# Kernel tuning notes

Hardware: AMD Instinct MI355X
Metric: run time of the kernel (lower is better)

The kernel has to match this reference:

```python
import jax, jax.numpy as jnp
import numpy as np

B, S, E, H = 2, 2048, 1024, 16
D = E // H  # head_dim = 64
NEG = -1e10


def setup_inputs() -> dict:
    key = jax.random.key(0)
    ks = jax.random.split(key, 12)
    sc = 1.0 / np.sqrt(E)
    return {
        "query": jax.random.normal(ks[0], (B, S, E), jnp.float32),
        "key_": jax.random.normal(ks[1], (B, S, E), jnp.float32),
        "value": jax.random.normal(ks[2], (B, S, E), jnp.float32),
        "mask": jax.random.randint(ks[3], (B, S), 0, 2, jnp.int32),
        "Wq": jax.random.normal(ks[4], (E, E), jnp.float32) * sc,
        "bq": jnp.zeros((E,), jnp.float32),
        "Wk": jax.random.normal(ks[5], (E, E), jnp.float32) * sc,
        "bk": jnp.zeros((E,), jnp.float32),
        "Wv": jax.random.normal(ks[6], (E, E), jnp.float32) * sc,
        "bv": jnp.zeros((E,), jnp.float32),
        "Wo": jax.random.normal(ks[7], (E, E), jnp.float32) * sc,
        "bo": jnp.zeros((E,), jnp.float32),
    }


def reference(query, key_, value, mask, Wq, bq, Wk, bk, Wv, bv, Wo, bo):
    # Linear projections (torch Linear: x @ W^T + b)
    Q = (query @ Wq.T + bq).reshape(B, S, H, D)
    K = (key_ @ Wk.T + bk).reshape(B, S, H, D)
    V = (value @ Wv.T + bv).reshape(B, S, H, D)
    # [B, H, Sq, Sk] scores
    scores = jnp.einsum("bqhd,bkhd->bhqk", Q, K) / jnp.sqrt(jnp.float32(D))
    # Original sets rows of masked query positions AND columns of masked key
    # positions to -1e10 (set, not add; overlapping assignment is same value).
    pad = (mask == 0)  # [B, S]
    bad = pad[:, :, None] | pad[:, None, :]  # [B, Sq, Sk]
    scores = scores + jnp.where(bad, NEG, 0.0)[:, None, :, :]
    weights = jax.nn.softmax(scores, axis=-1)
    out = jnp.einsum("bhqk,bkhd->bqhd", weights, V).reshape(B, S, E)
    return out @ Wo.T + bo
```

## Files before the change

### kernel.cpp

```cpp
#include <hip/hip_runtime.h>

typedef __attribute__((ext_vector_type(4)))  float          f32x4;
typedef __attribute__((ext_vector_type(16))) float          f32x16;
typedef __attribute__((ext_vector_type(8)))  short          s16x8;
typedef __attribute__((ext_vector_type(4)))  unsigned short u16x4;
typedef __attribute__((ext_vector_type(8)))  unsigned short u16x8;

#define MFMA_BF16(a, b, c) __builtin_amdgcn_mfma_f32_16x16x32_bf16((a), (b), (c), 0, 0, 0)
#define MFMA32(a, b, c)    __builtin_amdgcn_mfma_f32_32x32x16_bf16((a), (b), (c), 0, 0, 0)

static constexpr int Bb = 2, Ss = 2048, Ee = 1024, Hh = 16, Dd = 64;
static constexpr size_t M4 = 4u * 1024 * 1024;
static constexpr size_t M1 = 1024 * 1024;

__device__ __forceinline__ unsigned short f2b(float f) {
    unsigned u = __builtin_bit_cast(unsigned, f);
    u += 0x7fffu + ((u >> 16) & 1u);
    return (unsigned short)(u >> 16);
}

__device__ __forceinline__ void gld_lds16(const unsigned short* g, unsigned short* l) {
    __builtin_amdgcn_global_load_lds(
        (const __attribute__((address_space(1))) unsigned int*)g,
        (__attribute__((address_space(3))) unsigned int*)l, 16, 0, 0);
}

struct CvtArgs { const float* src[7]; unsigned short* dst;
                 const int* mask; float* maskf; };

__global__ __launch_bounds__(256) void cvt_bf16(CvtArgs a)
{
    if (blockIdx.x == 8192) {
#pragma unroll
        for (int j = 0; j < 16; j++) {
            int idx = threadIdx.x + j * 256;
            a.maskf[idx] = a.mask[idx] ? 1.f : 0.f;
        }
        return;
    }
    size_t i = ((size_t)blockIdx.x * 256 + threadIdx.x) * 8;
    int seg; size_t off;
    if (i < 3 * M4) { seg = (int)(i / M4);     off = i % M4; }
    else            { size_t j = i - 3 * M4;
                      seg = 3 + (int)(j / M1); off = j % M1; }
    const float* s = a.src[seg] + off;
    f32x4 x0 = *(const f32x4*)s;
    f32x4 x1 = *(const f32x4*)(s + 4);
    u16x8 o = (u16x8){f2b(x0[0]), f2b(x0[1]), f2b(x0[2]), f2b(x0[3]),
                      f2b(x1[0]), f2b(x1[1]), f2b(x1[2]), f2b(x1[3])};
    *(u16x8*)(a.dst + i) = o;
}

template <int OUT_MODE>
__device__ __forceinline__ void gemm_bf16_body(const unsigned short* __restrict__ A,
                                               const unsigned short* __restrict__ W,
                                               const float* __restrict__ bias,
                                               void* __restrict__ Cv,
                                               int m0, int n0)
{
    __shared__ __align__(16) unsigned short Al[128 * 32];
    __shared__ __align__(16) unsigned short Bl[128 * 32];

    const int tid  = threadIdx.x;
    const int lane = tid & 63;
    const int wid  = tid >> 6;
    const int quad = lane >> 4;
    const int lr   = lane & 15;
    const int wr   = (wid >> 1) * 64;
    const int wc   = (wid & 1) * 64;

    const int srow = wid * 32 + (lane >> 2);
    const int sk8  = (lane & 3) * 8;
    const unsigned short* gA = A + (size_t)(m0 + srow) * 1024 + sk8;
    const unsigned short* gW = W + (size_t)(n0 + srow) * 1024 + sk8;
    unsigned short* lA = &Al[wid * 1024];
    unsigned short* lW = &Bl[wid * 1024];

    f32x4 acc[4][4];
#pragma unroll
    for (int i = 0; i < 4; i++)
#pragma unroll
        for (int j = 0; j < 4; j++) acc[i][j] = (f32x4){0.f, 0.f, 0.f, 0.f};

    for (int ks = 0; ks < 1024; ks += 32) {
        __syncthreads();
        gld_lds16(gA + ks,              lA);
        gld_lds16(gA + ks + 16 * 1024,  lA + 512);
        gld_lds16(gW + ks,              lW);
        gld_lds16(gW + ks + 16 * 1024,  lW + 512);
        __syncthreads();

        s16x8 af[4], bf[4];
#pragma unroll
        for (int t = 0; t < 4; t++) {
            af[t] = *(const s16x8*)&Al[(wr + t * 16 + lr) * 32 + quad * 8];
            bf[t] = *(const s16x8*)&Bl[(wc + t * 16 + lr) * 32 + quad * 8];
        }
#pragma unroll
        for (int mt = 0; mt < 4; mt++)
#pragma unroll
            for (int nt = 0; nt < 4; nt++)
                acc[mt][nt] = MFMA_BF16(af[mt], bf[nt], acc[mt][nt]);
    }

#pragma unroll
    for (int mt = 0; mt < 4; mt++)
#pragma unroll
        for (int nt = 0; nt < 4; nt++) {
            int   col  = n0 + wc + nt * 16 + lr;
            float bcol = bias[col];
            int   rbase = m0 + wr + mt * 16 + quad * 4;
            if (OUT_MODE == 2) {
                int bb = rbase >> 11, s = rbase & 2047;
                u16x4 pk;
#pragma unroll
                for (int r = 0; r < 4; r++) pk[r] = f2b(acc[mt][nt][r] + bcol);
                *(u16x4*)&((unsigned short*)Cv)[((size_t)(bb * 1024 + col)) * 2048 + s] = pk;
            } else {
#pragma unroll
                for (int r = 0; r < 4; r++) {
                    float v = acc[mt][nt][r] + bcol;
                    if (OUT_MODE == 3) v *= 0.180336884f;
                    ((unsigned short*)Cv)[(size_t)(rbase + r) * 1024 + col] = f2b(v);
                }
            }
        }
}

struct GArgs {
    const unsigned short* A[3];
    const unsigned short* W[3];
    const float* bias[3];
    unsigned short* C[3];
};

__global__ __launch_bounds__(256) void proj_gemm(GArgs ga)
{
    const int id  = blockIdx.x;
    const int xcd = id & 7;
    const int t   = id >> 3;
    const int z   = t >> 5;
    const int tt  = t & 31;
    const int n0  = (tt & 7) * 128;
    const int m0  = (xcd * 4 + (tt >> 3)) * 128;

    if (z == 2)      gemm_bf16_body<2>(ga.A[2], ga.W[2], ga.bias[2], ga.C[2], m0, n0);
    else if (z == 1) gemm_bf16_body<1>(ga.A[1], ga.W[1], ga.bias[1], ga.C[1], m0, n0);
    else             gemm_bf16_body<3>(ga.A[0], ga.W[0], ga.bias[0], ga.C[0], m0, n0);
}

__global__ __launch_bounds__(256)
void out_gemm(const unsigned short* __restrict__ A,
              const unsigned short* __restrict__ W,
              const float* __restrict__ bias,
              float* __restrict__ C)
{
    __shared__ __align__(16) unsigned short Al[128 * 32];
    __shared__ __align__(16) unsigned short Bl[64 * 32];

    const int id  = blockIdx.x;
    const int xcd = id & 7;
    const int t   = id >> 3;
    const int n0  = (t & 15) * 64;
    const int m0  = (xcd * 4 + (t >> 4)) * 128;

    const int tid  = threadIdx.x;
    const int lane = tid & 63;
    const int wid  = tid >> 6;
    const int quad = lane >> 4;
    const int lr   = lane & 15;
    const int wr   = (wid >> 1) * 64;
    const int wc   = (wid & 1) * 32;

    const int srowA = wid * 32 + (lane >> 2);
    const int srowW = wid * 16 + (lane >> 2);
    const int sk8   = (lane & 3) * 8;
    const unsigned short* gA = A + (size_t)(m0 + srowA) * 1024 + sk8;
    const unsigned short* gW = W + (size_t)(n0 + srowW) * 1024 + sk8;
    unsigned short* lA = &Al[wid * 1024];
    unsigned short* lW = &Bl[wid * 512];

    f32x4 acc[4][2];
#pragma unroll
    for (int i = 0; i < 4; i++)
#pragma unroll
        for (int j = 0; j < 2; j++) acc[i][j] = (f32x4){0.f, 0.f, 0.f, 0.f};

    for (int ks = 0; ks < 1024; ks += 32) {
        __syncthreads();
        gld_lds16(gA + ks,              lA);
        gld_lds16(gA + ks + 16 * 1024,  lA + 512);
        gld_lds16(gW + ks,              lW);
        __syncthreads();

        s16x8 af[4], bf[2];
#pragma unroll
        for (int mt = 0; mt < 4; mt++)
            af[mt] = *(const s16x8*)&Al[(wr + mt * 16 + lr) * 32 + quad * 8];
#pragma unroll
        for (int nt = 0; nt < 2; nt++)
            bf[nt] = *(const s16x8*)&Bl[(wc + nt * 16 + lr) * 32 + quad * 8];
#pragma unroll
        for (int mt = 0; mt < 4; mt++)
#pragma unroll
            for (int nt = 0; nt < 2; nt++)
                acc[mt][nt] = MFMA_BF16(af[mt], bf[nt], acc[mt][nt]);
    }

#pragma unroll
    for (int mt = 0; mt < 4; mt++)
#pragma unroll
        for (int nt = 0; nt < 2; nt++) {
            int   col  = n0 + wc + nt * 16 + lr;
            float bcol = bias[col];
            int   rbase = m0 + wr + mt * 16 + quad * 4;
#pragma unroll
            for (int r = 0; r < 4; r++)
                C[(size_t)(rbase + r) * 1024 + col] = acc[mt][nt][r] + bcol;
        }
}

__global__ __launch_bounds__(256)
void flash_attn(const unsigned short* __restrict__ Q,
                const unsigned short* __restrict__ K,
                const unsigned short* __restrict__ Vt,
                const float* __restrict__ maskf,
                unsigned short* __restrict__ O)
{
    constexpr int   ST  = 76;
    constexpr float EPS = 9.31322575e-10f;
    __shared__ __align__(16) unsigned short Kl[64 * ST];
    __shared__ __align__(16) unsigned short Vl[64 * ST];
    __shared__ __align__(16) unsigned short Pl[64 * ST];
    __shared__ float lsq[4][32];

    const int id    = blockIdx.x;
    const int xcd   = id & 7;
    const int local = id >> 3;
    const int pair  = xcd * 4 + (local >> 5);
    const int b     = pair >> 4;
    const int h     = pair & 15;
    const int q0    = (local & 31) * 64;

    const int tid  = threadIdx.x;
    const int lane = tid & 63;
    const int wid  = tid >> 6;
    const int l31  = lane & 31;
    const int hl   = lane >> 5;
    const int qh   = wid & 1;
    const int kh   = wid >> 1;

    const unsigned short* qg =
        Q + (size_t)(b * 2048 + q0 + qh * 32 + l31) * 1024 + h * 64 + hl * 8;
    s16x8 qf[4];
#pragma unroll
    for (int db = 0; db < 4; db++) qf[db] = *(const s16x8*)(qg + db * 16);

    const float  mq  = maskf[b * 2048 + q0 + qh * 32 + l31];
    const float* mkp = maskf + b * 2048;

    const int lk = (tid >> 3) * ST + (tid & 7) * 8;
    const unsigned short* gK = K  + (size_t)(b * 2048 + (tid >> 3)) * 1024 + h * 64 + (tid & 7) * 8;
    const unsigned short* gV = Vt + (size_t)(b * 1024 + h * 64 + (tid >> 3)) * 2048 + (tid & 7) * 8;

    float  lsum = 0.f;
    f32x16 accO = (f32x16){0.f,0.f,0.f,0.f,0.f,0.f,0.f,0.f,
                           0.f,0.f,0.f,0.f,0.f,0.f,0.f,0.f};

    for (int kt = 0; kt < 2048; kt += 64) {
        __syncthreads();
        *(u16x8*)&Kl[lk]           = *(const u16x8*)(gK + (size_t)kt * 1024);
        *(u16x8*)&Kl[lk + 32 * ST] = *(const u16x8*)(gK + (size_t)(kt + 32) * 1024);
        *(u16x8*)&Vl[lk]           = *(const u16x8*)(gV + kt);
        *(u16x8*)&Vl[lk + 32 * ST] = *(const u16x8*)(gV + kt + (size_t)32 * 2048);
        __syncthreads();

        f32x16 st = (f32x16){0.f,0.f,0.f,0.f,0.f,0.f,0.f,0.f,
                             0.f,0.f,0.f,0.f,0.f,0.f,0.f,0.f};
#pragma unroll
        for (int db = 0; db < 4; db++) {
            s16x8 kf = *(const s16x8*)&Kl[(kh * 32 + l31) * ST + db * 16 + hl * 8];
            st = MFMA32(kf, qf[db], st);
        }
#pragma unroll
        for (int rq = 0; rq < 4; rq++) {
            int   kb = 4 * hl + 8 * rq;
            f32x4 m4 = *(const f32x4*)&mkp[kt + kh * 32 + kb];
            unsigned u[4];
#pragma unroll
            for (int r = 0; r < 4; r++) {
                float e = __builtin_amdgcn_exp2f(st[rq * 4 + r]);
                float p = e * (m4[r] * mq) + EPS;
                lsum += p;
                u[r] = __builtin_bit_cast(unsigned, p) + 0x8000u;
            }
            uint2 w;
            w.x = __builtin_amdgcn_perm(u[1], u[0], 0x07060302u);
            w.y = __builtin_amdgcn_perm(u[3], u[2], 0x07060302u);
            *(uint2*)&Pl[(qh * 32 + l31) * ST + kh * 32 + kb] = w;
        }
        __syncthreads();

#pragma unroll
        for (int ks = 0; ks < 4; ks++) {
            s16x8 pf = *(const s16x8*)&Pl[(qh * 32 + l31) * ST + ks * 16 + hl * 8];
            s16x8 vf = *(const s16x8*)&Vl[(kh * 32 + l31) * ST + ks * 16 + hl * 8];
            accO = MFMA32(pf, vf, accO);
        }
    }

    lsum += __shfl_xor(lsum, 32, 64);
    lsq[wid][l31] = lsum;
    __syncthreads();

#pragma unroll
    for (int rq = 0; rq < 4; rq++) {
        int   qr = 4 * hl + 8 * rq;
        f32x4 lA = *(const f32x4*)&lsq[qh][qr];
        f32x4 lB = *(const f32x4*)&lsq[qh + 2][qr];
#pragma unroll
        for (int r = 0; r < 4; r++) {
            float val = accO[rq * 4 + r] * __builtin_amdgcn_rcpf(lA[r] + lB[r]);
            O[(size_t)(b * 2048 + q0 + qh * 32 + qr + r) * 1024 + h * 64 +
              kh * 32 + l31] = f2b(val);
        }
    }
}

extern "C" void kernel_launch(void* const* d_in, const int* in_sizes, int n_in,
                              void* d_out, int out_size, void* d_ws, size_t ws_size,
                              hipStream_t stream)
{
    const float* query = (const float*)d_in[0];
    const float* key_  = (const float*)d_in[1];
    const float* value = (const float*)d_in[2];
    const int*   mask  = (const int*)d_in[3];
    const float* Wq    = (const float*)d_in[4];
    const float* bq    = (const float*)d_in[5];
    const float* Wk    = (const float*)d_in[6];
    const float* bk    = (const float*)d_in[7];
    const float* Wv    = (const float*)d_in[8];
    const float* bv    = (const float*)d_in[9];
    const float* Wo    = (const float*)d_in[10];
    const float* bo    = (const float*)d_in[11];
    float* out = (float*)d_out;

    unsigned short* cvt = (unsigned short*)d_ws;
    unsigned short* Aq  = cvt;
    unsigned short* Ak  = cvt + M4;
    unsigned short* Av  = cvt + 2 * M4;
    unsigned short* Wqb = cvt + 3 * M4;
    unsigned short* Wkb = Wqb + M1;
    unsigned short* Wvb = Wkb + M1;
    unsigned short* Wob = Wvb + M1;
    unsigned short* Qb  = Wob + M1;
    unsigned short* Kb  = Qb + M4;
    unsigned short* Vt  = Kb + M4;
    unsigned short* Ab  = Vt + M4;
    float*          mkf = (float*)(Ab + M4);

    CvtArgs ca;
    ca.src[0] = query; ca.src[1] = key_; ca.src[2] = value;
    ca.src[3] = Wq; ca.src[4] = Wk; ca.src[5] = Wv; ca.src[6] = Wo;
    ca.dst = cvt; ca.mask = mask; ca.maskf = mkf;
    cvt_bf16<<<dim3(8193), 256, 0, stream>>>(ca);

    GArgs ga;
    ga.A[0] = Aq;  ga.A[1] = Ak;  ga.A[2] = Av;
    ga.W[0] = Wqb; ga.W[1] = Wkb; ga.W[2] = Wvb;
    ga.bias[0] = bq; ga.bias[1] = bk; ga.bias[2] = bv;
    ga.C[0] = Qb; ga.C[1] = Kb; ga.C[2] = Vt;
    proj_gemm<<<dim3(768), 256, 0, stream>>>(ga);

    flash_attn<<<dim3(1024), 256, 0, stream>>>(Qb, Kb, Vt, mkf, Ab);
    out_gemm<<<dim3(512), 256, 0, stream>>>(Ab, Wob, bo, out);
}
```

Measured before the change: 234.7 us.

## Load K/V attention fragments directly from global into registers, bypassing LDS

```diff
diff --git a/kernel.cpp b/kernel.cpp
--- a/kernel.cpp
+++ b/kernel.cpp
@@ -229,8 +229,6 @@
 {
     constexpr int   ST  = 76;
     constexpr float EPS = 9.31322575e-10f;
-    __shared__ __align__(16) unsigned short Kl[64 * ST];
-    __shared__ __align__(16) unsigned short Vl[64 * ST];
     __shared__ __align__(16) unsigned short Pl[64 * ST];
     __shared__ float lsq[4][32];
 
@@ -259,29 +257,39 @@
     const float  mq  = maskf[b * 2048 + q0 + qh * 32 + l31];
     const float* mkp = maskf + b * 2048;
 
-    const int lk = (tid >> 3) * ST + (tid & 7) * 8;
-    const unsigned short* gK = K  + (size_t)(b * 2048 + (tid >> 3)) * 1024 + h * 64 + (tid & 7) * 8;
-    const unsigned short* gV = Vt + (size_t)(b * 1024 + h * 64 + (tid >> 3)) * 2048 + (tid & 7) * 8;
+    const unsigned short* gK2 =
+        K + (size_t)(b * 2048 + kh * 32 + l31) * 1024 + h * 64 + hl * 8;
+    const unsigned short* gV2 =
+        Vt + (size_t)(b * 1024 + h * 64 + kh * 32 + l31) * 2048 + hl * 8;
+
+    const int prow = (qh * 32 + l31) * ST;
 
     float  lsum = 0.f;
     f32x16 accO = (f32x16){0.f,0.f,0.f,0.f,0.f,0.f,0.f,0.f,
                            0.f,0.f,0.f,0.f,0.f,0.f,0.f,0.f};
 
+    s16x8 kf[4];
+#pragma unroll
+    for (int db = 0; db < 4; db++)
+        kf[db] = *(const s16x8*)(gK2 + db * 16);
+
     for (int kt = 0; kt < 2048; kt += 64) {
-        __syncthreads();
-        *(u16x8*)&Kl[lk]           = *(const u16x8*)(gK + (size_t)kt * 1024);
-        *(u16x8*)&Kl[lk + 32 * ST] = *(const u16x8*)(gK + (size_t)(kt + 32) * 1024);
-        *(u16x8*)&Vl[lk]           = *(const u16x8*)(gV + kt);
-        *(u16x8*)&Vl[lk + 32 * ST] = *(const u16x8*)(gV + kt + (size_t)32 * 2048);
-        __syncthreads();
-
         f32x16 st = (f32x16){0.f,0.f,0.f,0.f,0.f,0.f,0.f,0.f,
                              0.f,0.f,0.f,0.f,0.f,0.f,0.f,0.f};
 #pragma unroll
-        for (int db = 0; db < 4; db++) {
-            s16x8 kf = *(const s16x8*)&Kl[(kh * 32 + l31) * ST + db * 16 + hl * 8];
-            st = MFMA32(kf, qf[db], st);
-        }
+        for (int db = 0; db < 4; db++)
+            st = MFMA32(kf[db], qf[db], st);
+
+        if (kt + 64 < 2048) {
+#pragma unroll
+            for (int db = 0; db < 4; db++)
+                kf[db] = *(const s16x8*)(gK2 + (size_t)(kt + 64) * 1024 + db * 16);
+        }
+        s16x8 vf[4];
+#pragma unroll
+        for (int ks = 0; ks < 4; ks++)
+            vf[ks] = *(const s16x8*)(gV2 + kt + ks * 16);
+
 #pragma unroll
         for (int rq = 0; rq < 4; rq++) {
             int   kb = 4 * hl + 8 * rq;
@@ -297,16 +305,16 @@
             uint2 w;
             w.x = __builtin_amdgcn_perm(u[1], u[0], 0x07060302u);
             w.y = __builtin_amdgcn_perm(u[3], u[2], 0x07060302u);
-            *(uint2*)&Pl[(qh * 32 + l31) * ST + kh * 32 + kb] = w;
+            *(uint2*)&Pl[prow + kh * 32 + kb] = w;
         }
         __syncthreads();
 
 #pragma unroll
         for (int ks = 0; ks < 4; ks++) {
-            s16x8 pf = *(const s16x8*)&Pl[(qh * 32 + l31) * ST + ks * 16 + hl * 8];
-            s16x8 vf = *(const s16x8*)&Vl[(kh * 32 + l31) * ST + ks * 16 + hl * 8];
-            accO = MFMA32(pf, vf, accO);
-        }
+            s16x8 pf = *(const s16x8*)&Pl[prow + ks * 16 + hl * 8];
+            accO = MFMA32(pf, vf[ks], accO);
+        }
+        __syncthreads();
     }
 
     lsum += __shfl_xor(lsum, 32, 64);
```

Measured after the change: 323.5 us. +37.8%, slower.
